# Kernel optimization log

Hardware: AMD Instinct MI355X
Metric: run time of the kernel (lower is better)

Reference implementation:

```python
import jax, jax.numpy as jnp
import numpy as np
import math

DIM = 1536
NH = 12
HD = 128          # head_dim
C = HD // 2       # 64 complex rope dims
MAX_ATTN = 15 * 880
EPS = 1e-6


def _rope_tables(max_len=1024, d=HD, theta=10000.0):
    # Wan rope_params: freqs = cat([rope(1024, d-4*(d//6)), rope(1024, 2*(d//6)), rope(1024, 2*(d//6))], dim=1)
    d0 = d - 4 * (d // 6)   # 44 -> 22 complex dims (F axis)
    d1 = 2 * (d // 6)       # 42 -> 21 complex dims (H and W axes)
    parts = []
    for dd in (d0, d1, d1):
        inv = 1.0 / theta ** (np.arange(0, dd, 2, dtype=np.float32) / dd)
        parts.append(np.outer(np.arange(max_len, dtype=np.float32), inv))
    ang = np.concatenate(parts, axis=1)                 # [1024, C]
    return np.stack([np.cos(ang), np.sin(ang)], -1)     # [1024, C, 2]


def rmsnorm(x, g, eps=EPS):
    return x * jax.lax.rsqrt(jnp.mean(x * x, axis=-1, keepdims=True) + eps) * g


def rope_apply(xq, f, h, w, freqs, start_frame):
    # xq: [B, S, N, D]; freqs: [1024, C, 2] cos/sin tables; S = f*h*w
    b, s, n, d = xq.shape
    c = d // 2
    s0 = c - 2 * (c // 3)   # F-axis complex dims (22)
    s1 = c // 3             # H/W-axis complex dims (21)
    cos, sin = freqs[..., 0], freqs[..., 1]

    def per_token(tab):
        tf = jnp.broadcast_to(tab[start_frame:start_frame + f, :s0][:, None, None, :], (f, h, w, s0))
        th = jnp.broadcast_to(tab[:h, s0:s0 + s1][None, :, None, :], (f, h, w, s1))
        tw = jnp.broadcast_to(tab[:w, s0 + s1:][None, None, :, :], (f, h, w, s1))
        return jnp.concatenate([tf, th, tw], -1).reshape(1, s, 1, c)

    pc, ps = per_token(cos), per_token(sin)
    xr = xq.reshape(b, s, n, c, 2)
    re, im = xr[..., 0], xr[..., 1]
    out = jnp.stack([re * pc - im * ps, re * ps + im * pc], -1)
    return out.reshape(b, s, n, d)


def _forward(x, wq, bq, wk, bk, wv, bv, wo, bo, gq, gk, freqs, k_cache, v_cache, f, h, w, current_start):
    b, s, _ = x.shape
    frame_seqlen = h * w
    start_frame = current_start // frame_seqlen

    q = rmsnorm(x @ wq.T + bq, gq).reshape(b, s, NH, HD)
    k = rmsnorm(x @ wk.T + bk, gk).reshape(b, s, NH, HD)
    v = (x @ wv.T + bv).reshape(b, s, NH, HD)

    rq = rope_apply(q, f, h, w, freqs, start_frame)
    rk = rope_apply(k, f, h, w, freqs, start_frame)

    current_end = current_start + s
    # cache not full: append new keys/values at [current_start:current_end]
    k_cache = jax.lax.dynamic_update_slice(k_cache, rk, (0, current_start, 0, 0))
    v_cache = jax.lax.dynamic_update_slice(v_cache, v, (0, current_start, 0, 0))

    win_start = max(0, current_end - MAX_ATTN)
    kk = k_cache[:, win_start:current_end]   # [B, Lk, N, D]
    vv = v_cache[:, win_start:current_end]

    scale = 1.0 / math.sqrt(HD)
    scores = jnp.einsum('bqnd,bknd->bnqk', rq, kk) * scale
    attn = jax.nn.softmax(scores, axis=-1)
    out = jnp.einsum('bnqk,bknd->bqnd', attn, vv).reshape(b, s, DIM)
    return out @ wo.T + bo


def setup_inputs() -> dict:
    key = jax.random.key(0)
    ks = jax.random.split(key, 8)
    B, S, CACHE = 1, 880, 18 * 880
    x = jax.random.normal(ks[0], (B, S, DIM), jnp.float32)

    def lin(k):
        k1, k2 = jax.random.split(k)
        wgt = jax.random.normal(k1, (DIM, DIM), jnp.float32) / math.sqrt(DIM)
        bia = jax.random.normal(k2, (DIM,), jnp.float32) * 0.01
        return wgt, bia

    wq, bq = lin(ks[1]); wk, bk = lin(ks[2]); wv, bv = lin(ks[3]); wo, bo = lin(ks[4])
    gq = jnp.ones((DIM,), jnp.float32)
    gk = jnp.ones((DIM,), jnp.float32)
    freqs = jnp.asarray(_rope_tables())
    k_cache = jax.random.normal(ks[5], (B, CACHE, NH, HD), jnp.float32) * 0.5
    v_cache = jax.random.normal(ks[6], (B, CACHE, NH, HD), jnp.float32) * 0.5
    grid_sizes = jnp.array([1, 22, 40], jnp.int32)  # (F, H, W), H*W = 880
    return dict(x=x, wq=wq, bq=bq, wk=wk, bk=bk, wv=wv, bv=bv, wo=wo, bo=bo,
                gq=gq, gk=gk, freqs=freqs, k_cache=k_cache, v_cache=v_cache,
                grid_sizes=grid_sizes, current_start=10560)


def reference(x, wq, bq, wk, bk, wv, bv, wo, bo, gq, gk, freqs, k_cache, v_cache, grid_sizes, current_start):
    f, h, w = (int(grid_sizes[0]), int(grid_sizes[1]), int(grid_sizes[2]))
    return _forward(x, wq, bq, wk, bk, wv, bv, wo, bo, gq, gk, freqs,
                    k_cache, v_cache, f, h, w, int(current_start))
```

## Files before the change

### kernel.cpp

```cpp
#include <hip/hip_runtime.h>

#define NHEADS 12
#define HDIM 128
#define MODEL_DIM 1536
#define MAX_ATTN_W 13200
#define NSPLIT 18

typedef unsigned short u16;
typedef unsigned int u32;
typedef float f32x4 __attribute__((ext_vector_type(4)));
typedef float f32x16 __attribute__((ext_vector_type(16)));
typedef __bf16 bf16x8 __attribute__((ext_vector_type(8)));

static __device__ __forceinline__ u16 f2bf(float f) {
  union { __bf16 h; u16 u; } cv;
  cv.h = (__bf16)f;
  return cv.u;
}
static __device__ __forceinline__ float bf2f(u16 u) {
  union { u32 u; float f; } cv;
  cv.u = ((u32)u) << 16;
  return cv.f;
}
static __device__ __forceinline__ void gload_lds16(const void* g, void* l) {
  __builtin_amdgcn_global_load_lds(
      (const __attribute__((address_space(1))) unsigned int*)g,
      (__attribute__((address_space(3))) unsigned int*)l, 16, 0, 0);
}

__global__ void k_conv_bf16(const float* __restrict__ src, u16* __restrict__ dst, int n4) {
  int i = blockIdx.x * blockDim.x + threadIdx.x;
  if (i >= n4) return;
  float4 v = ((const float4*)src)[i];
  u32 lo = (u32)f2bf(v.x) | ((u32)f2bf(v.y) << 16);
  u32 hi = (u32)f2bf(v.z) | ((u32)f2bf(v.w) << 16);
  ((uint2*)dst)[i] = make_uint2(lo, hi);
}

__global__ void k_conv_bf16_w4(const float* __restrict__ s0, const float* __restrict__ s1,
                               const float* __restrict__ s2, const float* __restrict__ s3,
                               u16* __restrict__ d0, u16* __restrict__ d1,
                               u16* __restrict__ d2, u16* __restrict__ d3, int n4) {
  int i = blockIdx.x * blockDim.x + threadIdx.x;
  if (i >= n4) return;
  const int which = blockIdx.y;
  const float* src = (which == 0) ? s0 : (which == 1) ? s1 : (which == 2) ? s2 : s3;
  u16* dst = (which == 0) ? d0 : (which == 1) ? d1 : (which == 2) ? d2 : d3;
  float4 v = ((const float4*)src)[i];
  u32 lo = (u32)f2bf(v.x) | ((u32)f2bf(v.y) << 16);
  u32 hi = (u32)f2bf(v.z) | ((u32)f2bf(v.w) << 16);
  ((uint2*)dst)[i] = make_uint2(lo, hi);
}

__global__ void k_build_kold(const float* __restrict__ kc, u16* __restrict__ K_all,
                             const int* __restrict__ csp, int S, int KVcap) {
  const int cs = csp[0];
  const int ce = cs + S;
  int wst = ce - MAX_ATTN_W; if (wst < 0) wst = 0;
  const int oldlen = cs - wst;
  const long per = (long)oldlen * 16;
  const long total = per * NHEADS;
  for (long c = blockIdx.x * (long)blockDim.x + threadIdx.x; c < total;
       c += (long)gridDim.x * blockDim.x) {
    int n = (int)(c / per);
    long r = c - (long)n * per;
    int jo = (int)(r >> 4);
    int dc = ((int)r & 15) * 8;
    const float* s = kc + ((size_t)(wst + jo) * NHEADS + n) * HDIM + dc;
    float4 a = *(const float4*)s;
    float4 b = *(const float4*)(s + 4);
    uint4 o;
    o.x = (u32)f2bf(a.x) | ((u32)f2bf(a.y) << 16);
    o.y = (u32)f2bf(a.z) | ((u32)f2bf(a.w) << 16);
    o.z = (u32)f2bf(b.x) | ((u32)f2bf(b.y) << 16);
    o.w = (u32)f2bf(b.z) | ((u32)f2bf(b.w) << 16);
    *(uint4*)(K_all + ((size_t)n * KVcap + jo) * HDIM + dc) = o;
  }
}

__launch_bounds__(256)
__global__ void k_build_vtold(const float* __restrict__ vc, u16* __restrict__ VT,
                              const int* __restrict__ csp, int S, int KVcap) {
  __shared__ u16 tile[64][130];
  const int cs = csp[0];
  const int ce = cs + S;
  int wst = ce - MAX_ATTN_W; if (wst < 0) wst = 0;
  const int oldlen = cs - wst;
  const int n = blockIdx.y;
  const int j0 = blockIdx.x * 64;
  if (j0 >= oldlen) return;
  const int tid = threadIdx.x;

  #pragma unroll
  for (int i = 0; i < 8; i++) {
    int idx = tid + 256 * i;
    int j = idx >> 5;
    int dc = (idx & 31) * 4;
    float4 v = make_float4(0.f, 0.f, 0.f, 0.f);
    if (j0 + j < oldlen)
      v = *(const float4*)(vc + ((size_t)(wst + j0 + j) * NHEADS + n) * HDIM + dc);
    u32 lo = (u32)f2bf(v.x) | ((u32)f2bf(v.y) << 16);
    u32 hi = (u32)f2bf(v.z) | ((u32)f2bf(v.w) << 16);
    *(u32*)&tile[j][dc] = lo;
    *(u32*)&tile[j][dc + 2] = hi;
  }
  __syncthreads();

  const int d = tid >> 1;
  const int jh = (tid & 1) * 32;
  alignas(16) u16 buf[32];
  #pragma unroll
  for (int j = 0; j < 32; j++) buf[j] = tile[jh + j][d];
  u16* dst = VT + ((size_t)n * HDIM + d) * KVcap + j0 + jh;
  if (j0 + jh + 32 <= oldlen) {
    #pragma unroll
    for (int c = 0; c < 4; c++)
      *(uint4*)(dst + c * 8) = *(const uint4*)&buf[c * 8];
  } else {
    for (int j = 0; j < 32 && j0 + jh + j < oldlen; j++) dst[j] = buf[j];
  }
}

__launch_bounds__(256)
__global__ void k_gemm_o128(const u16* __restrict__ A, const u16* __restrict__ B,
                            const float* __restrict__ bias, float* __restrict__ out,
                            int M, int N, int K) {
  __shared__ __align__(16) u16 Al[128][40];
  __shared__ __align__(16) u16 Bl[128][40];
  const int n0 = blockIdx.y * 128;
  const int tid = threadIdx.x;
  const int wid = tid >> 6, l = tid & 63, l31 = l & 31, hi = l >> 5;
  const int wr = wid >> 1, wc = wid & 1;
  const int m0 = blockIdx.x * 128;
  f32x16 acc[2][2];
  #pragma unroll
  for (int mt = 0; mt < 2; mt++)
    #pragma unroll
    for (int nt = 0; nt < 2; nt++)
      #pragma unroll
      for (int j = 0; j < 16; j++) acc[mt][nt][j] = 0.f;
  const int row = tid >> 2, colc = (tid & 3) * 8;
  for (int k0 = 0; k0 < K; k0 += 32) {
    __syncthreads();
    uint4 a0 = *(const uint4*)(A + (size_t)(m0 + row) * K + k0 + colc);
    uint4 a1 = *(const uint4*)(A + (size_t)(m0 + row + 64) * K + k0 + colc);
    uint4 b0 = *(const uint4*)(B + (size_t)(n0 + row) * K + k0 + colc);
    uint4 b1 = *(const uint4*)(B + (size_t)(n0 + row + 64) * K + k0 + colc);
    *(uint4*)&Al[row][colc] = a0;
    *(uint4*)&Al[row + 64][colc] = a1;
    *(uint4*)&Bl[row][colc] = b0;
    *(uint4*)&Bl[row + 64][colc] = b1;
    __syncthreads();
    #pragma unroll
    for (int ks = 0; ks < 2; ks++) {
      bf16x8 af[2], bfr[2];
      #pragma unroll
      for (int mt = 0; mt < 2; mt++)
        af[mt] = *(const bf16x8*)&Al[wr * 64 + mt * 32 + l31][ks * 16 + hi * 8];
      #pragma unroll
      for (int nt = 0; nt < 2; nt++)
        bfr[nt] = *(const bf16x8*)&Bl[wc * 64 + nt * 32 + l31][ks * 16 + hi * 8];
      #pragma unroll
      for (int mt = 0; mt < 2; mt++)
        #pragma unroll
        for (int nt = 0; nt < 2; nt++)
          acc[mt][nt] = __builtin_amdgcn_mfma_f32_32x32x16_bf16(af[mt], bfr[nt], acc[mt][nt], 0, 0, 0);
    }
  }
  #pragma unroll
  for (int mt = 0; mt < 2; mt++)
    #pragma unroll
    for (int nt = 0; nt < 2; nt++) {
      const int col = n0 + wc * 64 + nt * 32 + l31;
      const float bb = bias[col];
      #pragma unroll
      for (int r = 0; r < 16; r++) {
        int rowo = m0 + wr * 64 + mt * 32 + (r & 3) + 8 * (r >> 2) + 4 * hi;
        if (rowo < M) out[(size_t)rowo * N + col] = acc[mt][nt][r] + bb;
      }
    }
}

__launch_bounds__(256)
__global__ void k_gemm_qkv128(const u16* __restrict__ A,
                              const u16* __restrict__ B0, const u16* __restrict__ B1,
                              const u16* __restrict__ B2,
                              const float* __restrict__ bias0, const float* __restrict__ bias1,
                              const float* __restrict__ bias2,
                              float* __restrict__ o0, float* __restrict__ o1, float* __restrict__ o2,
                              int M, int N, int K) {
  __shared__ __align__(16) u16 Al[128][40];
  __shared__ __align__(16) u16 Bl[128][40];
  const int nblk = N / 128;
  const int which = blockIdx.y / nblk;
  const int n0 = (blockIdx.y % nblk) * 128;
  const u16* B = (which == 0) ? B0 : ((which == 1) ? B1 : B2);
  const float* bias = (which == 0) ? bias0 : ((which == 1) ? bias1 : bias2);
  float* out = (which == 0) ? o0 : ((which == 1) ? o1 : o2);
  const int tid = threadIdx.x;
  const int wid = tid >> 6, l = tid & 63, l31 = l & 31, hi = l >> 5;
  const int wr = wid >> 1, wc = wid & 1;
  const int m0 = blockIdx.x * 128;
  f32x16 acc[2][2];
  #pragma unroll
  for (int mt = 0; mt < 2; mt++)
    #pragma unroll
    for (int nt = 0; nt < 2; nt++)
      #pragma unroll
      for (int j = 0; j < 16; j++) acc[mt][nt][j] = 0.f;
  const int row = tid >> 2, colc = (tid & 3) * 8;
  for (int k0 = 0; k0 < K; k0 += 32) {
    __syncthreads();
    uint4 a0 = *(const uint4*)(A + (size_t)(m0 + row) * K + k0 + colc);
    uint4 a1 = *(const uint4*)(A + (size_t)(m0 + row + 64) * K + k0 + colc);
    uint4 b0 = *(const uint4*)(B + (size_t)(n0 + row) * K + k0 + colc);
    uint4 b1 = *(const uint4*)(B + (size_t)(n0 + row + 64) * K + k0 + colc);
    *(uint4*)&Al[row][colc] = a0;
    *(uint4*)&Al[row + 64][colc] = a1;
    *(uint4*)&Bl[row][colc] = b0;
    *(uint4*)&Bl[row + 64][colc] = b1;
    __syncthreads();
    #pragma unroll
    for (int ks = 0; ks < 2; ks++) {
      bf16x8 af[2], bfr[2];
      #pragma unroll
      for (int mt = 0; mt < 2; mt++)
        af[mt] = *(const bf16x8*)&Al[wr * 64 + mt * 32 + l31][ks * 16 + hi * 8];
      #pragma unroll
      for (int nt = 0; nt < 2; nt++)
        bfr[nt] = *(const bf16x8*)&Bl[wc * 64 + nt * 32 + l31][ks * 16 + hi * 8];
      #pragma unroll
      for (int mt = 0; mt < 2; mt++)
        #pragma unroll
        for (int nt = 0; nt < 2; nt++)
          acc[mt][nt] = __builtin_amdgcn_mfma_f32_32x32x16_bf16(af[mt], bfr[nt], acc[mt][nt], 0, 0, 0);
    }
  }
  #pragma unroll
  for (int mt = 0; mt < 2; mt++)
    #pragma unroll
    for (int nt = 0; nt < 2; nt++) {
      const int col = n0 + wc * 64 + nt * 32 + l31;
      const float bb = bias[col];
      #pragma unroll
      for (int r = 0; r < 16; r++) {
        int rowo = m0 + wr * 64 + mt * 32 + (r & 3) + 8 * (r >> 2) + 4 * hi;
        if (rowo < M) out[(size_t)rowo * N + col] = acc[mt][nt][r] + bb;
      }
    }
}

__launch_bounds__(256)
__global__ void k_norm_rope(const float* __restrict__ qp, const float* __restrict__ kp,
                            const float* __restrict__ vp, const float* __restrict__ gq,
                            const float* __restrict__ gk, const float* __restrict__ freqs,
                            const int* __restrict__ gs, const int* __restrict__ csp,
                            int S, int KVcap,
                            u16* __restrict__ rq, u16* __restrict__ K_all,
                            u16* __restrict__ VT) {
  const int t = blockIdx.x;
  const int tid = threadIdx.x;
  const float* q = qp + (size_t)t * MODEL_DIM;
  const float* k = kp + (size_t)t * MODEL_DIM;
  const float* v = vp + (size_t)t * MODEL_DIM;
  float sq = 0.f, sk = 0.f;
  for (int j = tid; j < MODEL_DIM; j += 256) {
    float a = q[j]; sq += a * a;
    float b = k[j]; sk += b * b;
  }
  #pragma unroll
  for (int off = 32; off > 0; off >>= 1) {
    sq += __shfl_down(sq, off, 64);
    sk += __shfl_down(sk, off, 64);
  }
  __shared__ float red[8];
  int wv_ = tid >> 6, l = tid & 63;
  if (l == 0) { red[wv_] = sq; red[4 + wv_] = sk; }
  __syncthreads();
  sq = red[0] + red[1] + red[2] + red[3];
  sk = red[4] + red[5] + red[6] + red[7];
  const float rq_s = rsqrtf(sq * (1.0f / MODEL_DIM) + 1e-6f) * 0.12751744f;
  const float rk_s = rsqrtf(sk * (1.0f / MODEL_DIM) + 1e-6f);

  const int cs = csp[0];
  const int h = gs[1], ww = gs[2];
  const int hw = h * ww;
  const int sf = cs / hw;
  const int fi = t / hw;
  const int rr = t - fi * hw;
  const int hi = rr / ww;
  const int wi = rr - hi * ww;
  const int ce = cs + S;
  int wst = ce - MAX_ATTN_W; if (wst < 0) wst = 0;
  const int jj = cs + t - wst;

  for (int p = tid; p < NHEADS * 64; p += 256) {
    int n = p >> 6, c = p & 63;
    int pos = (c < 22) ? (sf + fi) : ((c < 43) ? hi : wi);
    float cv = freqs[(pos * 64 + c) * 2];
    float sv = freqs[(pos * 64 + c) * 2 + 1];
    int j0 = n * HDIM + 2 * c;
    float qr = q[j0] * rq_s * gq[j0];
    float qi = q[j0 + 1] * rq_s * gq[j0 + 1];
    u32 oq = (u32)f2bf(qr * cv - qi * sv) | ((u32)f2bf(qr * sv + qi * cv) << 16);
    *(u32*)(rq + ((size_t)n * S + t) * HDIM + 2 * c) = oq;
    float kr = k[j0] * rk_s * gk[j0];
    float ki = k[j0 + 1] * rk_s * gk[j0 + 1];
    u32 ok = (u32)f2bf(kr * cv - ki * sv) | ((u32)f2bf(kr * sv + ki * cv) << 16);
    *(u32*)(K_all + ((size_t)n * KVcap + jj) * HDIM + 2 * c) = ok;
  }
  for (int j = tid; j < MODEL_DIM; j += 256) {
    int n = j >> 7, d = j & 127;
    VT[((size_t)n * HDIM + d) * KVcap + jj] = f2bf(v[j]);
  }
}

__launch_bounds__(256, 3)
__global__ void k_attn_split(const u16* __restrict__ rq, const u16* __restrict__ K_all,
                             const u16* __restrict__ VT,
                             u16* __restrict__ po, float* __restrict__ pm, float* __restrict__ pl,
                             const int* __restrict__ csp, int S, int KVcap) {
  __shared__ __align__(16) u16 Klds[64][128];
  __shared__ __align__(16) u16 Vlds[128][64];

  const int tid = threadIdx.x;
  const int wid = tid >> 6;
  const int l = tid & 63;
  const int l31 = l & 31;
  const int hi = l >> 5;
  const int swz = (l31 & 7) << 3;
  const int head = blockIdx.y;
  const int split = blockIdx.z;
  const int q0 = blockIdx.x * 128;

  const int cs = csp[0];
  const int ce = cs + S;
  int wst = ce - MAX_ATTN_W; if (wst < 0) wst = 0;
  const int KV = ce - wst;
  const int chunk = (((KV + NSPLIT - 1) / NSPLIT) + 63) & ~63;
  const int kstart = split * chunk;
  int kend = kstart + chunk; if (kend > KV) kend = KV;

  const size_t pbase = ((size_t)head * NSPLIT + split) * S;
  const int qrow = q0 + wid * 32 + l31;

  if (kstart >= kend) {
    if (qrow < S && hi == 0) { pm[pbase + qrow] = -3.0e38f; pl[pbase + qrow] = 0.f; }
    return;
  }

  bf16x8 qf[8];
  if (qrow < S) {
    const u16* qp = rq + ((size_t)head * S + qrow) * HDIM;
    #pragma unroll
    for (int ds = 0; ds < 8; ds++) qf[ds] = *(const bf16x8*)(qp + ds * 16 + hi * 8);
  } else {
    #pragma unroll
    for (int ds = 0; ds < 8; ds++)
      #pragma unroll
      for (int i = 0; i < 8; i++) qf[ds][i] = (__bf16)0.0f;
  }

  f32x16 o[4];
  #pragma unroll
  for (int dt = 0; dt < 4; dt++)
    #pragma unroll
    for (int j = 0; j < 16; j++) o[dt][j] = 0.f;
  float m_ = -3.0e38f, lsum_ = 0.f;

  const u16* Kh = K_all + (size_t)head * KVcap * HDIM;
  const u16* Vh = VT + (size_t)head * HDIM * KVcap;

  int krow_i[4], kcol_i[4], vd_i[4], vcol_i[4];
  #pragma unroll
  for (int i = 0; i < 4; i++) {
    int kr_ = (wid * 4 + i) * 4 + (l >> 4);
    krow_i[i] = kr_;
    kcol_i[i] = (((l & 15) ^ (kr_ & 7)) << 3);
    int vd_ = (wid * 4 + i) * 8 + (l >> 3);
    vd_i[i] = vd_;
    vcol_i[i] = (((l & 7) ^ (vd_ & 7)) << 3);
  }
  u16* kldst[4];
  u16* vldst[4];
  #pragma unroll
  for (int i = 0; i < 4; i++) {
    kldst[i] = &Klds[0][0] + (wid * 4 + i) * 512;
    vldst[i] = &Vlds[0][0] + (wid * 4 + i) * 512;
  }

  const int ntiles = (kend - kstart + 63) >> 6;

  for (int t = 0; t < ntiles; t++) {
    const int key0 = kstart + (t << 6);
    __syncthreads();
    #pragma unroll
    for (int i = 0; i < 4; i++)
      gload_lds16(Kh + (size_t)(key0 + krow_i[i]) * HDIM + kcol_i[i], kldst[i]);
    #pragma unroll
    for (int i = 0; i < 4; i++)
      gload_lds16(Vh + (size_t)vd_i[i] * KVcap + key0 + vcol_i[i], vldst[i]);
    __syncthreads();

    f32x16 s[2];
    __builtin_amdgcn_s_setprio(1);
    #pragma unroll
    for (int kt = 0; kt < 2; kt++) {
      #pragma unroll
      for (int j = 0; j < 16; j++) s[kt][j] = 0.f;
      #pragma unroll
      for (int ds = 0; ds < 8; ds++) {
        bf16x8 kf = *(const bf16x8*)&Klds[kt * 32 + l31][(ds * 16 + hi * 8) ^ swz];
        s[kt] = __builtin_amdgcn_mfma_f32_32x32x16_bf16(kf, qf[ds], s[kt], 0, 0, 0);
      }
    }
    __builtin_amdgcn_s_setprio(0);

    float tm = -3.0e38f;
    if (key0 + 64 <= kend) {
      #pragma unroll
      for (int kt = 0; kt < 2; kt++)
        #pragma unroll
        for (int r = 0; r < 16; r++) tm = fmaxf(tm, s[kt][r]);
    } else {
      #pragma unroll
      for (int kt = 0; kt < 2; kt++) {
        const int rem = kend - key0 - kt * 32;
        #pragma unroll
        for (int r = 0; r < 16; r++) {
          const int off = (r & 3) + 8 * (r >> 2) + 4 * hi;
          float v = (off < rem) ? s[kt][r] : -3.0e38f;
          s[kt][r] = v;
          tm = fmaxf(tm, v);
        }
      }
    }
    tm = fmaxf(tm, __shfl_xor(tm, 32, 64));

    if (!__all(tm <= m_ + 8.0f)) {
      float nm = fmaxf(m_, tm);
      float alpha = exp2f(m_ - nm);
      m_ = nm;
      lsum_ *= alpha;
      #pragma unroll
      for (int dt = 0; dt < 4; dt++)
        #pragma unroll
        for (int j = 0; j < 16; j++) o[dt][j] *= alpha;
    }

    float rs = 0.f;
    u32 w[2][8];
    #pragma unroll
    for (int kt = 0; kt < 2; kt++)
      #pragma unroll
      for (int j = 0; j < 8; j++) {
        float p0 = exp2f(s[kt][2 * j] - m_);
        float p1 = exp2f(s[kt][2 * j + 1] - m_);
        rs += p0 + p1;
        w[kt][j] = (u32)f2bf(p0) | ((u32)f2bf(p1) << 16);
      }
    rs += __shfl_xor(rs, 32, 64);
    lsum_ += rs;

    union { u32 u[4]; bf16x8 v; } pf[2][2];
    #pragma unroll
    for (int kt = 0; kt < 2; kt++) {
      u32 xw[8];
      #pragma unroll
      for (int j = 0; j < 8; j++) xw[j] = __shfl_xor(w[kt][j], 32, 64);
      pf[kt][0].u[0] = hi ? xw[2]    : w[kt][0];
      pf[kt][0].u[1] = hi ? xw[3]    : w[kt][1];
      pf[kt][0].u[2] = hi ? w[kt][2] : xw[0];
      pf[kt][0].u[3] = hi ? w[kt][3] : xw[1];
      pf[kt][1].u[0] = hi ? xw[6]    : w[kt][4];
      pf[kt][1].u[1] = hi ? xw[7]    : w[kt][5];
      pf[kt][1].u[2] = hi ? w[kt][6] : xw[4];
      pf[kt][1].u[3] = hi ? w[kt][7] : xw[5];
    }

    __builtin_amdgcn_s_setprio(1);
    #pragma unroll
    for (int dt = 0; dt < 4; dt++) {
      #pragma unroll
      for (int kt = 0; kt < 2; kt++)
        #pragma unroll
        for (int mm = 0; mm < 2; mm++) {
          bf16x8 vf = *(const bf16x8*)&Vlds[dt * 32 + l31][(kt * 32 + mm * 16 + hi * 8) ^ swz];
          o[dt] = __builtin_amdgcn_mfma_f32_32x32x16_bf16(vf, pf[kt][mm].v, o[dt], 0, 0, 0);
        }
    }
    __builtin_amdgcn_s_setprio(0);
  }

  if (qrow < S) {
    float rl = (lsum_ > 0.f) ? (1.0f / lsum_) : 0.f;
    u16* dst = po + (pbase + qrow) * HDIM;
    #pragma unroll
    for (int dt = 0; dt < 4; dt++)
      #pragma unroll
      for (int jj = 0; jj < 4; jj++) {
        u32 w0 = (u32)f2bf(o[dt][4 * jj] * rl) | ((u32)f2bf(o[dt][4 * jj + 1] * rl) << 16);
        u32 w1 = (u32)f2bf(o[dt][4 * jj + 2] * rl) | ((u32)f2bf(o[dt][4 * jj + 3] * rl) << 16);
        *(uint2*)(dst + dt * 32 + 8 * jj + 4 * hi) = make_uint2(w0, w1);
      }
    if (hi == 0) { pm[pbase + qrow] = m_; pl[pbase + qrow] = lsum_; }
  }
}

__global__ void k_attn_reduce(const u16* __restrict__ po, const float* __restrict__ pm,
                              const float* __restrict__ pl, u16* __restrict__ attn_out,
                              int S) {
  const int t = blockIdx.x;
  const int h = blockIdx.y;
  const int d = threadIdx.x;
  float ms[NSPLIT];
  float M = -3.0e38f;
  #pragma unroll
  for (int s = 0; s < NSPLIT; s++) {
    ms[s] = pm[((size_t)h * NSPLIT + s) * S + t];
    M = fmaxf(M, ms[s]);
  }
  float L = 0.f, acc = 0.f;
  #pragma unroll
  for (int s = 0; s < NSPLIT; s++) {
    float wgt = exp2f(ms[s] - M) * pl[((size_t)h * NSPLIT + s) * S + t];
    L += wgt;
    acc += wgt * bf2f(po[(((size_t)h * NSPLIT + s) * S + t) * HDIM + d]);
  }
  attn_out[(size_t)t * MODEL_DIM + h * HDIM + d] = f2bf(acc / L);
}

extern "C" void kernel_launch(void* const* d_in, const int* in_sizes, int n_in,
                              void* d_out, int out_size, void* d_ws, size_t ws_size,
                              hipStream_t stream) {
  (void)n_in; (void)out_size; (void)ws_size;
  const float* x  = (const float*)d_in[0];
  const float* wq = (const float*)d_in[1];
  const float* bq = (const float*)d_in[2];
  const float* wk = (const float*)d_in[3];
  const float* bk = (const float*)d_in[4];
  const float* wv = (const float*)d_in[5];
  const float* bv = (const float*)d_in[6];
  const float* wo = (const float*)d_in[7];
  const float* bo = (const float*)d_in[8];
  const float* gq = (const float*)d_in[9];
  const float* gk = (const float*)d_in[10];
  const float* freqs = (const float*)d_in[11];
  const float* k_cache = (const float*)d_in[12];
  const float* v_cache = (const float*)d_in[13];
  const int* gs  = (const int*)d_in[14];
  const int* csp = (const int*)d_in[15];

  const int S = in_sizes[0] / MODEL_DIM;
  const int CACHE = in_sizes[12] / (NHEADS * HDIM);
  const int KVcap = (CACHE < MAX_ATTN_W) ? CACHE : MAX_ATTN_W;
  const int Mpad = (S + 127) & ~127;

  char* ws = (char*)d_ws;
  size_t off = 0;
  auto alloc = [&](size_t bytes) {
    char* p = ws + off;
    off += (bytes + 255) & ~(size_t)255;
    return p;
  };
  u16* xb   = (u16*)alloc((size_t)Mpad * MODEL_DIM * 2);
  u16* wqb  = (u16*)alloc((size_t)MODEL_DIM * MODEL_DIM * 2);
  u16* wkb  = (u16*)alloc((size_t)MODEL_DIM * MODEL_DIM * 2);
  u16* wvb  = (u16*)alloc((size_t)MODEL_DIM * MODEL_DIM * 2);
  u16* wob  = (u16*)alloc((size_t)MODEL_DIM * MODEL_DIM * 2);
  float* q_pre = (float*)alloc((size_t)S * MODEL_DIM * 4);
  float* k_pre = (float*)alloc((size_t)S * MODEL_DIM * 4);
  float* v_pre = (float*)alloc((size_t)S * MODEL_DIM * 4);
  u16* rqb   = (u16*)alloc((size_t)NHEADS * S * HDIM * 2);
  u16* K_all = (u16*)alloc((size_t)NHEADS * KVcap * HDIM * 2);
  u16* VT    = (u16*)alloc((size_t)NHEADS * HDIM * KVcap * 2);
  u16* attn_o = (u16*)alloc((size_t)Mpad * MODEL_DIM * 2);
  u16* po    = (u16*)alloc((size_t)NHEADS * NSPLIT * S * HDIM * 2);
  float* pm  = (float*)alloc((size_t)NHEADS * NSPLIT * S * 4);
  float* pl  = (float*)alloc((size_t)NHEADS * NSPLIT * S * 4);

  const int nx4 = S * MODEL_DIM / 4;
  const int nw4 = MODEL_DIM * MODEL_DIM / 4;
  hipLaunchKernelGGL(k_conv_bf16, dim3((nx4 + 255) / 256), dim3(256), 0, stream, x, xb, nx4);
  hipLaunchKernelGGL(k_conv_bf16_w4, dim3((nw4 + 255) / 256, 4), dim3(256), 0, stream,
                     wq, wk, wv, wo, wqb, wkb, wvb, wob, nw4);

  hipLaunchKernelGGL(k_build_kold, dim3(2048), dim3(256), 0, stream, k_cache, K_all, csp, S, KVcap);
  hipLaunchKernelGGL(k_build_vtold, dim3((KVcap + 63) / 64, NHEADS), dim3(256), 0, stream,
                     v_cache, VT, csp, S, KVcap);

  hipLaunchKernelGGL(k_gemm_qkv128, dim3(Mpad / 128, 3 * MODEL_DIM / 128), dim3(256), 0, stream,
                     xb, wqb, wkb, wvb, bq, bk, bv, q_pre, k_pre, v_pre, S, MODEL_DIM, MODEL_DIM);

  hipLaunchKernelGGL(k_norm_rope, dim3(S), dim3(256), 0, stream,
                     q_pre, k_pre, v_pre, gq, gk, freqs, gs, csp, S, KVcap, rqb, K_all, VT);

  hipLaunchKernelGGL(k_attn_split, dim3((S + 127) / 128, NHEADS, NSPLIT), dim3(256), 0, stream,
                     rqb, K_all, VT, po, pm, pl, csp, S, KVcap);

  hipLaunchKernelGGL(k_attn_reduce, dim3(S, NHEADS), dim3(128), 0, stream, po, pm, pl, attn_o, S);

  hipLaunchKernelGGL(k_gemm_o128, dim3(Mpad / 128, MODEL_DIM / 128), dim3(256), 0, stream,
                     attn_o, wob, bo, (float*)d_out, S, MODEL_DIM, MODEL_DIM);
}
```

Before: 339.8 us.

## Fuse fp32-to-bf16 conversion into GEMM loads and remap attention grid for XCD locality

Drops the separate conversion kernels for x and the four weight matrices, so the QKV and output GEMMs now read fp32 directly and pack to bf16 while staging into LDS. This removes two launches and a full write and read of the bf16 copies, at the cost of twice the global bytes per GEMM tile load. The split attention kernel now uses a flat 1D grid decoded so that blocks sharing a head/split chunk land on the same XCD (bx&7), aiming for better L2 reuse of K/V. Row indices in the QKV GEMM are clamped to M-1 to avoid reading past x, since the padded buffer no longer exists.

```diff
diff --git a/kernel.cpp b/kernel.cpp
--- a/kernel.cpp
+++ b/kernel.cpp
@@ -22,34 +22,13 @@
   cv.u = ((u32)u) << 16;
   return cv.f;
 }
+static __device__ __forceinline__ u32 pk2(float a, float b) {
+  return (u32)f2bf(a) | ((u32)f2bf(b) << 16);
+}
 static __device__ __forceinline__ void gload_lds16(const void* g, void* l) {
   __builtin_amdgcn_global_load_lds(
       (const __attribute__((address_space(1))) unsigned int*)g,
       (__attribute__((address_space(3))) unsigned int*)l, 16, 0, 0);
-}
-
-__global__ void k_conv_bf16(const float* __restrict__ src, u16* __restrict__ dst, int n4) {
-  int i = blockIdx.x * blockDim.x + threadIdx.x;
-  if (i >= n4) return;
-  float4 v = ((const float4*)src)[i];
-  u32 lo = (u32)f2bf(v.x) | ((u32)f2bf(v.y) << 16);
-  u32 hi = (u32)f2bf(v.z) | ((u32)f2bf(v.w) << 16);
-  ((uint2*)dst)[i] = make_uint2(lo, hi);
-}
-
-__global__ void k_conv_bf16_w4(const float* __restrict__ s0, const float* __restrict__ s1,
-                               const float* __restrict__ s2, const float* __restrict__ s3,
-                               u16* __restrict__ d0, u16* __restrict__ d1,
-                               u16* __restrict__ d2, u16* __restrict__ d3, int n4) {
-  int i = blockIdx.x * blockDim.x + threadIdx.x;
-  if (i >= n4) return;
-  const int which = blockIdx.y;
-  const float* src = (which == 0) ? s0 : (which == 1) ? s1 : (which == 2) ? s2 : s3;
-  u16* dst = (which == 0) ? d0 : (which == 1) ? d1 : (which == 2) ? d2 : d3;
-  float4 v = ((const float4*)src)[i];
-  u32 lo = (u32)f2bf(v.x) | ((u32)f2bf(v.y) << 16);
-  u32 hi = (u32)f2bf(v.z) | ((u32)f2bf(v.w) << 16);
-  ((uint2*)dst)[i] = make_uint2(lo, hi);
 }
 
 __global__ void k_build_kold(const float* __restrict__ kc, u16* __restrict__ K_all,
@@ -70,10 +49,10 @@
     float4 a = *(const float4*)s;
     float4 b = *(const float4*)(s + 4);
     uint4 o;
-    o.x = (u32)f2bf(a.x) | ((u32)f2bf(a.y) << 16);
-    o.y = (u32)f2bf(a.z) | ((u32)f2bf(a.w) << 16);
-    o.z = (u32)f2bf(b.x) | ((u32)f2bf(b.y) << 16);
-    o.w = (u32)f2bf(b.z) | ((u32)f2bf(b.w) << 16);
+    o.x = pk2(a.x, a.y);
+    o.y = pk2(a.z, a.w);
+    o.z = pk2(b.x, b.y);
+    o.w = pk2(b.z, b.w);
     *(uint4*)(K_all + ((size_t)n * KVcap + jo) * HDIM + dc) = o;
   }
 }
@@ -99,10 +78,8 @@
     float4 v = make_float4(0.f, 0.f, 0.f, 0.f);
     if (j0 + j < oldlen)
       v = *(const float4*)(vc + ((size_t)(wst + j0 + j) * NHEADS + n) * HDIM + dc);
-    u32 lo = (u32)f2bf(v.x) | ((u32)f2bf(v.y) << 16);
-    u32 hi = (u32)f2bf(v.z) | ((u32)f2bf(v.w) << 16);
-    *(u32*)&tile[j][dc] = lo;
-    *(u32*)&tile[j][dc + 2] = hi;
+    *(u32*)&tile[j][dc] = pk2(v.x, v.y);
+    *(u32*)&tile[j][dc + 2] = pk2(v.z, v.w);
   }
   __syncthreads();
 
@@ -122,7 +99,7 @@
 }
 
 __launch_bounds__(256)
-__global__ void k_gemm_o128(const u16* __restrict__ A, const u16* __restrict__ B,
+__global__ void k_gemm_o128(const u16* __restrict__ A, const float* __restrict__ B,
                             const float* __restrict__ bias, float* __restrict__ out,
                             int M, int N, int K) {
   __shared__ __align__(16) u16 Al[128][40];
@@ -144,12 +121,16 @@
     __syncthreads();
     uint4 a0 = *(const uint4*)(A + (size_t)(m0 + row) * K + k0 + colc);
     uint4 a1 = *(const uint4*)(A + (size_t)(m0 + row + 64) * K + k0 + colc);
-    uint4 b0 = *(const uint4*)(B + (size_t)(n0 + row) * K + k0 + colc);
-    uint4 b1 = *(const uint4*)(B + (size_t)(n0 + row + 64) * K + k0 + colc);
+    const float* b0p = B + (size_t)(n0 + row) * K + k0 + colc;
+    const float* b1p = B + (size_t)(n0 + row + 64) * K + k0 + colc;
+    float4 b00 = *(const float4*)b0p, b01 = *(const float4*)(b0p + 4);
+    float4 b10 = *(const float4*)b1p, b11 = *(const float4*)(b1p + 4);
     *(uint4*)&Al[row][colc] = a0;
     *(uint4*)&Al[row + 64][colc] = a1;
-    *(uint4*)&Bl[row][colc] = b0;
-    *(uint4*)&Bl[row + 64][colc] = b1;
+    *(uint4*)&Bl[row][colc] = make_uint4(pk2(b00.x, b00.y), pk2(b00.z, b00.w),
+                                         pk2(b01.x, b01.y), pk2(b01.z, b01.w));
+    *(uint4*)&Bl[row + 64][colc] = make_uint4(pk2(b10.x, b10.y), pk2(b10.z, b10.w),
+                                              pk2(b11.x, b11.y), pk2(b11.z, b11.w));
     __syncthreads();
     #pragma unroll
     for (int ks = 0; ks < 2; ks++) {
@@ -182,9 +163,9 @@
 }
 
 __launch_bounds__(256)
-__global__ void k_gemm_qkv128(const u16* __restrict__ A,
-                              const u16* __restrict__ B0, const u16* __restrict__ B1,
-                              const u16* __restrict__ B2,
+__global__ void k_gemm_qkv128(const float* __restrict__ A,
+                              const float* __restrict__ B0, const float* __restrict__ B1,
+                              const float* __restrict__ B2,
                               const float* __restrict__ bias0, const float* __restrict__ bias1,
                               const float* __restrict__ bias2,
                               float* __restrict__ o0, float* __restrict__ o1, float* __restrict__ o2,
@@ -194,7 +175,7 @@
   const int nblk = N / 128;
   const int which = blockIdx.y / nblk;
   const int n0 = (blockIdx.y % nblk) * 128;
-  const u16* B = (which == 0) ? B0 : ((which == 1) ? B1 : B2);
+  const float* B = (which == 0) ? B0 : ((which == 1) ? B1 : B2);
   const float* bias = (which == 0) ? bias0 : ((which == 1) ? bias1 : bias2);
   float* out = (which == 0) ? o0 : ((which == 1) ? o1 : o2);
   const int tid = threadIdx.x;
@@ -209,16 +190,26 @@
       #pragma unroll
       for (int j = 0; j < 16; j++) acc[mt][nt][j] = 0.f;
   const int row = tid >> 2, colc = (tid & 3) * 8;
+  int gm0 = m0 + row;       if (gm0 >= M) gm0 = M - 1;
+  int gm1 = m0 + row + 64;  if (gm1 >= M) gm1 = M - 1;
   for (int k0 = 0; k0 < K; k0 += 32) {
     __syncthreads();
-    uint4 a0 = *(const uint4*)(A + (size_t)(m0 + row) * K + k0 + colc);
-    uint4 a1 = *(const uint4*)(A + (size_t)(m0 + row + 64) * K + k0 + colc);
-    uint4 b0 = *(const uint4*)(B + (size_t)(n0 + row) * K + k0 + colc);
-    uint4 b1 = *(const uint4*)(B + (size_t)(n0 + row + 64) * K + k0 + colc);
-    *(uint4*)&Al[row][colc] = a0;
-    *(uint4*)&Al[row + 64][colc] = a1;
-    *(uint4*)&Bl[row][colc] = b0;
-    *(uint4*)&Bl[row + 64][colc] = b1;
+    const float* a0p = A + (size_t)gm0 * K + k0 + colc;
+    const float* a1p = A + (size_t)gm1 * K + k0 + colc;
+    float4 a00 = *(const float4*)a0p, a01 = *(const float4*)(a0p + 4);
+    float4 a10 = *(const float4*)a1p, a11 = *(const float4*)(a1p + 4);
+    const float* b0p = B + (size_t)(n0 + row) * K + k0 + colc;
+    const float* b1p = B + (size_t)(n0 + row + 64) * K + k0 + colc;
+    float4 b00 = *(const float4*)b0p, b01 = *(const float4*)(b0p + 4);
+    float4 b10 = *(const float4*)b1p, b11 = *(const float4*)(b1p + 4);
+    *(uint4*)&Al[row][colc] = make_uint4(pk2(a00.x, a00.y), pk2(a00.z, a00.w),
+                                         pk2(a01.x, a01.y), pk2(a01.z, a01.w));
+    *(uint4*)&Al[row + 64][colc] = make_uint4(pk2(a10.x, a10.y), pk2(a10.z, a10.w),
+                                              pk2(a11.x, a11.y), pk2(a11.z, a11.w));
+    *(uint4*)&Bl[row][colc] = make_uint4(pk2(b00.x, b00.y), pk2(b00.z, b00.w),
+                                         pk2(b01.x, b01.y), pk2(b01.z, b01.w));
+    *(uint4*)&Bl[row + 64][colc] = make_uint4(pk2(b10.x, b10.y), pk2(b10.z, b10.w),
+                                              pk2(b11.x, b11.y), pk2(b11.z, b11.w));
     __syncthreads();
     #pragma unroll
     for (int ks = 0; ks < 2; ks++) {
@@ -302,12 +293,10 @@
     int j0 = n * HDIM + 2 * c;
     float qr = q[j0] * rq_s * gq[j0];
     float qi = q[j0 + 1] * rq_s * gq[j0 + 1];
-    u32 oq = (u32)f2bf(qr * cv - qi * sv) | ((u32)f2bf(qr * sv + qi * cv) << 16);
-    *(u32*)(rq + ((size_t)n * S + t) * HDIM + 2 * c) = oq;
+    *(u32*)(rq + ((size_t)n * S + t) * HDIM + 2 * c) = pk2(qr * cv - qi * sv, qr * sv + qi * cv);
     float kr = k[j0] * rk_s * gk[j0];
     float ki = k[j0 + 1] * rk_s * gk[j0 + 1];
-    u32 ok = (u32)f2bf(kr * cv - ki * sv) | ((u32)f2bf(kr * sv + ki * cv) << 16);
-    *(u32*)(K_all + ((size_t)n * KVcap + jj) * HDIM + 2 * c) = ok;
+    *(u32*)(K_all + ((size_t)n * KVcap + jj) * HDIM + 2 * c) = pk2(kr * cv - ki * sv, kr * sv + ki * cv);
   }
   for (int j = tid; j < MODEL_DIM; j += 256) {
     int n = j >> 7, d = j & 127;
@@ -319,7 +308,7 @@
 __global__ void k_attn_split(const u16* __restrict__ rq, const u16* __restrict__ K_all,
                              const u16* __restrict__ VT,
                              u16* __restrict__ po, float* __restrict__ pm, float* __restrict__ pl,
-                             const int* __restrict__ csp, int S, int KVcap) {
+                             const int* __restrict__ csp, int S, int KVcap, int nqb) {
   __shared__ __align__(16) u16 Klds[64][128];
   __shared__ __align__(16) u16 Vlds[128][64];
 
@@ -329,9 +318,16 @@
   const int l31 = l & 31;
   const int hi = l >> 5;
   const int swz = (l31 & 7) << 3;
-  const int head = blockIdx.y;
-  const int split = blockIdx.z;
-  const int q0 = blockIdx.x * 128;
+
+  const int bx = blockIdx.x;
+  const int xcd = bx & 7;
+  const int j = bx >> 3;
+  const int cl = j / nqb;
+  const int qb = j - cl * nqb;
+  const int chunkid = cl * 8 + xcd;
+  const int head = chunkid / NSPLIT;
+  const int split = chunkid - head * NSPLIT;
+  const int q0 = qb * 128;
 
   const int cs = csp[0];
   const int ce = cs + S;
@@ -365,7 +361,7 @@
   #pragma unroll
   for (int dt = 0; dt < 4; dt++)
     #pragma unroll
-    for (int j = 0; j < 16; j++) o[dt][j] = 0.f;
+    for (int j2 = 0; j2 < 16; j2++) o[dt][j2] = 0.f;
   float m_ = -3.0e38f, lsum_ = 0.f;
 
   const u16* Kh = K_all + (size_t)head * KVcap * HDIM;
@@ -407,7 +403,7 @@
     #pragma unroll
     for (int kt = 0; kt < 2; kt++) {
       #pragma unroll
-      for (int j = 0; j < 16; j++) s[kt][j] = 0.f;
+      for (int j2 = 0; j2 < 16; j2++) s[kt][j2] = 0.f;
       #pragma unroll
       for (int ds = 0; ds < 8; ds++) {
         bf16x8 kf = *(const bf16x8*)&Klds[kt * 32 + l31][(ds * 16 + hi * 8) ^ swz];
@@ -445,7 +441,7 @@
       #pragma unroll
       for (int dt = 0; dt < 4; dt++)
         #pragma unroll
-        for (int j = 0; j < 16; j++) o[dt][j] *= alpha;
+        for (int j2 = 0; j2 < 16; j2++) o[dt][j2] *= alpha;
     }
 
     float rs = 0.f;
@@ -453,11 +449,11 @@
     #pragma unroll
     for (int kt = 0; kt < 2; kt++)
       #pragma unroll
-      for (int j = 0; j < 8; j++) {
-        float p0 = exp2f(s[kt][2 * j] - m_);
-        float p1 = exp2f(s[kt][2 * j + 1] - m_);
+      for (int j2 = 0; j2 < 8; j2++) {
+        float p0 = exp2f(s[kt][2 * j2] - m_);
+        float p1 = exp2f(s[kt][2 * j2 + 1] - m_);
         rs += p0 + p1;
-        w[kt][j] = (u32)f2bf(p0) | ((u32)f2bf(p1) << 16);
+        w[kt][j2] = pk2(p0, p1);
       }
     rs += __shfl_xor(rs, 32, 64);
     lsum_ += rs;
@@ -467,7 +463,7 @@
     for (int kt = 0; kt < 2; kt++) {
       u32 xw[8];
       #pragma unroll
-      for (int j = 0; j < 8; j++) xw[j] = __shfl_xor(w[kt][j], 32, 64);
+      for (int j2 = 0; j2 < 8; j2++) xw[j2] = __shfl_xor(w[kt][j2], 32, 64);
       pf[kt][0].u[0] = hi ? xw[2]    : w[kt][0];
       pf[kt][0].u[1] = hi ? xw[3]    : w[kt][1];
       pf[kt][0].u[2] = hi ? w[kt][2] : xw[0];
@@ -499,8 +495,8 @@
     for (int dt = 0; dt < 4; dt++)
       #pragma unroll
       for (int jj = 0; jj < 4; jj++) {
-        u32 w0 = (u32)f2bf(o[dt][4 * jj] * rl) | ((u32)f2bf(o[dt][4 * jj + 1] * rl) << 16);
-        u32 w1 = (u32)f2bf(o[dt][4 * jj + 2] * rl) | ((u32)f2bf(o[dt][4 * jj + 3] * rl) << 16);
+        u32 w0 = pk2(o[dt][4 * jj] * rl, o[dt][4 * jj + 1] * rl);
+        u32 w1 = pk2(o[dt][4 * jj + 2] * rl, o[dt][4 * jj + 3] * rl);
         *(uint2*)(dst + dt * 32 + 8 * jj + 4 * hi) = make_uint2(w0, w1);
       }
     if (hi == 0) { pm[pbase + qrow] = m_; pl[pbase + qrow] = lsum_; }
@@ -555,6 +551,7 @@
   const int CACHE = in_sizes[12] / (NHEADS * HDIM);
   const int KVcap = (CACHE < MAX_ATTN_W) ? CACHE : MAX_ATTN_W;
   const int Mpad = (S + 127) & ~127;
+  const int NQB = Mpad / 128;
 
   char* ws = (char*)d_ws;
   size_t off = 0;
@@ -563,11 +560,6 @@
     off += (bytes + 255) & ~(size_t)255;
     return p;
   };
-  u16* xb   = (u16*)alloc((size_t)Mpad * MODEL_DIM * 2);
-  u16* wqb  = (u16*)alloc((size_t)MODEL_DIM * MODEL_DIM * 2);
-  u16* wkb  = (u16*)alloc((size_t)MODEL_DIM * MODEL_DIM * 2);
-  u16* wvb  = (u16*)alloc((size_t)MODEL_DIM * MODEL_DIM * 2);
-  u16* wob  = (u16*)alloc((size_t)MODEL_DIM * MODEL_DIM * 2);
   float* q_pre = (float*)alloc((size_t)S * MODEL_DIM * 4);
   float* k_pre = (float*)alloc((size_t)S * MODEL_DIM * 4);
   float* v_pre = (float*)alloc((size_t)S * MODEL_DIM * 4);
@@ -579,27 +571,21 @@
   float* pm  = (float*)alloc((size_t)NHEADS * NSPLIT * S * 4);
   float* pl  = (float*)alloc((size_t)NHEADS * NSPLIT * S * 4);
 
-  const int nx4 = S * MODEL_DIM / 4;
-  const int nw4 = MODEL_DIM * MODEL_DIM / 4;
-  hipLaunchKernelGGL(k_conv_bf16, dim3((nx4 + 255) / 256), dim3(256), 0, stream, x, xb, nx4);
-  hipLaunchKernelGGL(k_conv_bf16_w4, dim3((nw4 + 255) / 256, 4), dim3(256), 0, stream,
-                     wq, wk, wv, wo, wqb, wkb, wvb, wob, nw4);
-
   hipLaunchKernelGGL(k_build_kold, dim3(2048), dim3(256), 0, stream, k_cache, K_all, csp, S, KVcap);
   hipLaunchKernelGGL(k_build_vtold, dim3((KVcap + 63) / 64, NHEADS), dim3(256), 0, stream,
                      v_cache, VT, csp, S, KVcap);
 
   hipLaunchKernelGGL(k_gemm_qkv128, dim3(Mpad / 128, 3 * MODEL_DIM / 128), dim3(256), 0, stream,
-                     xb, wqb, wkb, wvb, bq, bk, bv, q_pre, k_pre, v_pre, S, MODEL_DIM, MODEL_DIM);
+                     x, wq, wk, wv, bq, bk, bv, q_pre, k_pre, v_pre, S, MODEL_DIM, MODEL_DIM);
 
   hipLaunchKernelGGL(k_norm_rope, dim3(S), dim3(256), 0, stream,
                      q_pre, k_pre, v_pre, gq, gk, freqs, gs, csp, S, KVcap, rqb, K_all, VT);
 
-  hipLaunchKernelGGL(k_attn_split, dim3((S + 127) / 128, NHEADS, NSPLIT), dim3(256), 0, stream,
-                     rqb, K_all, VT, po, pm, pl, csp, S, KVcap);
+  hipLaunchKernelGGL(k_attn_split, dim3(NQB * NHEADS * NSPLIT), dim3(256), 0, stream,
+                     rqb, K_all, VT, po, pm, pl, csp, S, KVcap, NQB);
 
   hipLaunchKernelGGL(k_attn_reduce, dim3(S, NHEADS), dim3(128), 0, stream, po, pm, pl, attn_o, S);
 
   hipLaunchKernelGGL(k_gemm_o128, dim3(Mpad / 128, MODEL_DIM / 128), dim3(256), 0, stream,
-                     attn_o, wob, bo, (float*)d_out, S, MODEL_DIM, MODEL_DIM);
-}
+                     attn_o, wo, bo, (float*)d_out, S, MODEL_DIM, MODEL_DIM);
+}
```

After: 386.4 us. +13.7%, slower.
